# Performance work log

Measured on AMD Instinct MI355X. Metric: run time of the kernel, lower is better.

## Reference

```python
import jax, jax.numpy as jnp
from jax import lax
import numpy as np

B, C, O, K, H, W = 32, 64, 64, 3, 128, 128
COND = 16
DN = ('NCHW', 'OIHW', 'NCHW')


def setup_inputs() -> dict:
    key = jax.random.key(0)
    ks = jax.random.split(key, 12)
    def rn(k, shape, fan_in):
        return jax.random.normal(k, shape, dtype=jnp.float32) / np.sqrt(fan_in)
    return {
        "x": jax.random.normal(ks[0], (B, C, H, W), dtype=jnp.float32),
        # condition_generator: Conv2d(C,16,3,stride=2) -> pool -> relu -> Conv2d(16,16,1) -> relu
        "cg_w1": rn(ks[1], (COND, C, 3, 3), C * 9),
        "cg_b1": jnp.zeros((COND,), jnp.float32),
        "cg_w2": rn(ks[2], (COND, COND), COND),
        "cg_b2": jnp.zeros((COND,), jnp.float32),
        # weight_generator: Conv2d(16, C*K*K, 1) + ReLU
        "wg_w": rn(ks[3], (C * K * K, COND), COND),
        "wg_b": 0.1 * jax.random.normal(ks[4], (C * K * K,), dtype=jnp.float32),
        # pointwise_generator: Conv2d(16, C*O, 1) + ReLU  (channels viewed as [O, C])
        "pg_w": rn(ks[5], (C * O, COND), COND),
        "pg_b": 0.1 * jax.random.normal(ks[6], (C * O,), dtype=jnp.float32),
        # bias_generator: Conv2d(16, O, 1)
        "bg_w": rn(ks[7], (O, COND), COND),
        "bg_b": jnp.zeros((O,), jnp.float32),
        # BatchNorm2d(O) affine params (training-mode batch stats)
        "bn_gamma": jnp.ones((O,), jnp.float32),
        "bn_beta": jnp.zeros((O,), jnp.float32),
    }


def reference(x, cg_w1, cg_b1, cg_w2, cg_b2, wg_w, wg_b, pg_w, pg_b,
              bg_w, bg_b, bn_gamma, bn_beta):
    b, c, h, w = x.shape
    # ---- condition generator: conv3x3 s2 (VALID) -> global avgpool -> relu -> 1x1 -> relu
    cond = lax.conv_general_dilated(x, cg_w1, (2, 2), 'VALID', dimension_numbers=DN)
    cond = cond + cg_b1[None, :, None, None]
    cond = cond.mean(axis=(2, 3))                      # [B,16] (AdaptiveAvgPool2d(1))
    cond = jax.nn.relu(cond)
    cond = jax.nn.relu(cond @ cg_w2.T + cg_b2)         # [B,16]
    # ---- per-sample dynamic weights
    dw = jax.nn.relu(cond @ wg_w.T + wg_b).reshape(b, c, 1, K, K)   # depthwise [B,C,1,K,K]
    pw = jax.nn.relu(cond @ pg_w.T + pg_b).reshape(b, O, c)         # pointwise [B,O,C]
    dbias = cond @ bg_w.T + bg_b                                    # [B,O]
    # ---- per-sample depthwise conv (stride=1, padding=1), vmapped over batch
    def dwconv(xi, ki):  # xi [C,H,W], ki [C,1,K,K]
        return lax.conv_general_dilated(xi[None], ki, (1, 1), [(1, 1), (1, 1)],
                                        feature_group_count=c,
                                        dimension_numbers=DN)[0]
    y = jax.vmap(dwconv)(x, dw)                        # [B,C,H,W]
    # ---- per-sample pointwise 1x1 conv + dynamic bias
    out = jnp.einsum('bchw,boc->bohw', y, pw) + dbias[:, :, None, None]
    # ---- BatchNorm2d (training mode: batch statistics over N,H,W)
    mean = out.mean(axis=(0, 2, 3))
    var = out.var(axis=(0, 2, 3))
    out = (out - mean[None, :, None, None]) * lax.rsqrt(var[None, :, None, None] + 1e-5)
    out = out * bn_gamma[None, :, None, None] + bn_beta[None, :, None, None]
    return out
```

## Files before the change

kernel.cpp:

```cpp
#include <hip/hip_runtime.h>

#define B_ 32
#define C_ 64
#define O_ 64
#define H_ 128
#define W_ 128

typedef __attribute__((ext_vector_type(8))) short short8;
typedef __attribute__((ext_vector_type(4))) short short4v;
typedef __attribute__((ext_vector_type(4))) float f32x4;

typedef __attribute__((address_space(1))) const void gv_t;
typedef __attribute__((address_space(3))) void lv_t;

static __device__ __forceinline__ unsigned short f2bf(float f) {
    unsigned u = __builtin_bit_cast(unsigned, f);
    unsigned r = (u + 0x7FFFu + ((u >> 16) & 1u)) >> 16;
    return (unsigned short)r;
}

static __device__ __forceinline__ unsigned pk_bf16(float lo, float hi) {
    unsigned r;
    asm("v_cvt_pk_bf16_f32 %0, %1, %2" : "=v"(r) : "v"(lo), "v"(hi));
    return r;
}

#define WS_S      0
#define WS_COND2  18432
#define WS_DW     18944
#define WS_DBIAS  37376
#define WS_PWBF   39424
#define WS_PSUM   104960
#define WS_PSQ    236032
#define WS_SCALE  367104
#define WS_SHIFT  367168

__global__ void __launch_bounds__(256) k_strided_sums(const float* __restrict__ x,
                                                      float* __restrict__ Sout) {
    int t = threadIdx.x;
    int bc = blockIdx.x;
    const float4* xp = (const float4*)(x + (size_t)bc * (H_ * W_));
    float a[9];
#pragma unroll
    for (int k = 0; k < 9; k++) a[k] = 0.f;
#pragma unroll
    for (int k = 0; k < 16; k++) {
        int i4 = t + k * 256;
        int h = i4 >> 5;
        int w0 = (i4 & 31) << 2;
        float4 v = xp[i4];
        float mA = (w0 == 124) ? 0.f : 1.f;
        float mB = (w0 == 0) ? 0.f : 1.f;
        float rs0 = v.x + mA * v.z;
        float rs1 = v.y + mA * v.w;
        float rs2 = mB * v.x + v.z;
        float e  = (h & 1) ? 0.f : 1.f;
        float od = 1.f - e;
        float hm0 = (h == 126) ? 0.f : e;
        float hm2 = (h == 0)   ? 0.f : e;
        float hm1 = (h == 127) ? 0.f : od;
        a[0] = fmaf(hm0, rs0, a[0]); a[1] = fmaf(hm0, rs1, a[1]); a[2] = fmaf(hm0, rs2, a[2]);
        a[3] = fmaf(hm1, rs0, a[3]); a[4] = fmaf(hm1, rs1, a[4]); a[5] = fmaf(hm1, rs2, a[5]);
        a[6] = fmaf(hm2, rs0, a[6]); a[7] = fmaf(hm2, rs1, a[7]); a[8] = fmaf(hm2, rs2, a[8]);
    }
    __shared__ float red[4][9];
    int lane = t & 63, wv = t >> 6;
#pragma unroll
    for (int k = 0; k < 9; k++) {
        float v = a[k];
        for (int off = 32; off > 0; off >>= 1) v += __shfl_down(v, off);
        if (lane == 0) red[wv][k] = v;
    }
    __syncthreads();
    if (t < 9) Sout[(size_t)bc * 9 + t] = red[0][t] + red[1][t] + red[2][t] + red[3][t];
}

__global__ void __launch_bounds__(256) k_cond(const float* __restrict__ S,
                       const float* __restrict__ w1, const float* __restrict__ b1,
                       const float* __restrict__ w2, const float* __restrict__ b2,
                       float* __restrict__ cond2) {
    int b = blockIdx.x;
    int t = threadIdx.x;
    int j = t >> 4, seg = t & 15;
    const float* Sb = S + b * 576;
    const float* w1j = w1 + j * 576;
    int i0 = seg * 36;
    float s = 0.f;
#pragma unroll 4
    for (int i = 0; i < 36; i++) s = fmaf(Sb[i0 + i], w1j[i0 + i], s);
    __shared__ float red[16][16];
    __shared__ float condv[16];
    red[j][seg] = s;
    __syncthreads();
    if (t < 16) {
        float acc = 0.f;
#pragma unroll
        for (int k = 0; k < 16; k++) acc += red[t][k];
        acc = acc * (1.f / 3969.f) + b1[t];
        condv[t] = fmaxf(acc, 0.f);
    }
    __syncthreads();
    if (t < 16) {
        float s2 = b2[t];
#pragma unroll
        for (int k = 0; k < 16; k++) s2 = fmaf(condv[k], w2[t * 16 + k], s2);
        cond2[b * 16 + t] = fmaxf(s2, 0.f);
    }
}

__global__ void k_dyn(const float* __restrict__ cond2,
                      const float* __restrict__ wg_w, const float* __restrict__ wg_b,
                      const float* __restrict__ pg_w, const float* __restrict__ pg_b,
                      const float* __restrict__ bg_w, const float* __restrict__ bg_b,
                      float* __restrict__ dw, unsigned short* __restrict__ pwbf,
                      float* __restrict__ dbias) {
    int idx = blockIdx.x * 256 + threadIdx.x;
    if (idx < 18432) {
        int b = idx / 576, r = idx - b * 576;
        const float* cd = cond2 + b * 16;
        float s = wg_b[r];
#pragma unroll
        for (int j = 0; j < 16; j++) s += cd[j] * wg_w[r * 16 + j];
        dw[idx] = fmaxf(s, 0.f);
    } else if (idx < 18432 + 131072) {
        int k = idx - 18432;
        int b = k >> 12, r = k & 4095;
        const float* cd = cond2 + b * 16;
        float s = pg_b[r];
#pragma unroll
        for (int j = 0; j < 16; j++) s += cd[j] * pg_w[r * 16 + j];
        pwbf[k] = f2bf(fmaxf(s, 0.f));
    } else if (idx < 151552) {
        int k = idx - 149504;
        int b = k >> 6, r = k & 63;
        const float* cd = cond2 + b * 16;
        float s = bg_b[r];
#pragma unroll
        for (int j = 0; j < 16; j++) s += cd[j] * bg_w[r * 16 + j];
        dbias[k] = s;
    }
}

struct SM4 {
    unsigned short y[256 * 36];
    float xr[2][4][4][128];
    float dwl[64 * 12];
    float sred[4][64];
    float qred[4][64];
    float dbl[64];
};

__global__ void __launch_bounds__(256, 4) k_fused(
        const float* __restrict__ x, const float* __restrict__ dw,
        const unsigned short* __restrict__ pwbf, const float* __restrict__ dbias,
        float* __restrict__ out, float* __restrict__ psum, float* __restrict__ psq) {
    __shared__ SM4 sm;
    int t = threadIdx.x;
    int bx = blockIdx.x;
    int b = bx >> 6;
    int pt = bx & 63;
    int h0 = pt << 1;

    int l = t & 63, w_id = t >> 6;
    int quad = l >> 4, l15 = l & 15;
    int pxbase = w_id << 6;

    int m = t & 3;
    int px0 = t & ~3;
    int h_loc = px0 >> 7;
    int w0 = px0 & 127;
    float mk0 = (h0 == 0   && h_loc == 0) ? 0.f : 1.f;
    float mk2 = (h0 == 126 && h_loc == 1) ? 0.f : 1.f;

    for (int i = t; i < 576; i += 256) {
        int c = i / 9, k = i - c * 9;
        sm.dwl[c * 12 + k] = dw[b * 576 + i];
    }
    if (t < 64) sm.dbl[t] = dbias[b * 64 + t];

    const float* xb = x + ((size_t)b << 20);
    const unsigned short* pwb = pwbf + (size_t)b * 4096;

    f32x4 acc[4][4];
#pragma unroll
    for (int i = 0; i < 4; i++)
#pragma unroll
        for (int j = 0; j < 4; j++) acc[i][j] = (f32x4){0.f, 0.f, 0.f, 0.f};

    auto stage = [&](int bf, int cbg) {
#pragma unroll
        for (int k2 = 0; k2 < 2; k2++) {
            int f4 = t + k2 * 256;
            int cc = f4 >> 7, rem = f4 & 127;
            int rr = rem >> 5, w4 = rem & 31;
            int hh = h0 - 1 + rr;
            hh = hh < 0 ? 0 : (hh > 127 ? 127 : hh);
            const float* src = xb + ((size_t)(cbg + cc) << 14) + hh * 128 + (w4 << 2);
            float* dst = &sm.xr[bf][cc][rr][w4 << 2];
            __builtin_amdgcn_global_load_lds((gv_t*)src, (lv_t*)dst, 16, 0, 0);
        }
    };

    short8 bfr[4];
    auto load_bfr = [&](int hf) {
#pragma unroll
        for (int nt = 0; nt < 4; nt++) {
            int o = nt * 16 + l15;
            bfr[nt] = *(const short8*)(pwb + o * 64 + hf * 32 + quad * 8);
        }
    };

    auto domfma = [&]() {
        char* yb = (char*)sm.y;
#pragma unroll
        for (int mt = 0; mt < 4; mt++) {
            int px = pxbase + mt * 16 + l15;
            int bofs = px * 72;
            int sx = px & 7;
            short4v lo = *(short4v*)(yb + bofs + 8 * ((2 * quad)     ^ sx));
            short4v hi = *(short4v*)(yb + bofs + 8 * ((2 * quad + 1) ^ sx));
            short8 a = __builtin_shufflevector(lo, hi, 0, 1, 2, 3, 4, 5, 6, 7);
#pragma unroll
            for (int nt = 0; nt < 4; nt++)
                acc[mt][nt] = __builtin_amdgcn_mfma_f32_16x16x32_bf16(
                    a, bfr[nt], acc[mt][nt], 0, 0, 0);
        }
    };

    load_bfr(0);
    stage(0, 0);
    __syncthreads();

    int buf = 0;
#pragma unroll
    for (int idx = 0; idx < 16; idx++) {
        int cb = idx * 4;
        int rp = idx & 7;
        if (idx < 15) stage(buf ^ 1, cb + 4);

        const float* dvp = sm.dwl + (cb + m) * 12;
        float4 d0 = *(const float4*)(dvp);
        float4 d1 = *(const float4*)(dvp + 4);
        float4 d2 = *(const float4*)(dvp + 8);
        float dA0 = d0.x * mk0, dB0 = d0.y * mk0, dC0 = d0.z * mk0;
        float dA1 = d0.w,       dB1 = d1.x,       dC1 = d1.y;
        float dA2 = d1.z * mk2, dB2 = d1.w * mk2, dC2 = d2.x * mk2;
        const float* xc = &sm.xr[buf][m][0][0];
        float y0 = 0.f, y1 = 0.f, y2 = 0.f, y3 = 0.f;
#define STEN(dAx, dBx, dCx, KH) { \
        const float* row = xc + (h_loc + KH) * 128; \
        float4 fc = *(const float4*)(row + w0); \
        float4 fm = *(const float4*)(row + (w0 ? w0 - 4 : 0)); \
        float4 fp = *(const float4*)(row + ((w0 < 124) ? w0 + 4 : 120)); \
        float lft = w0 ? fm.w : 0.f; \
        float rgt = (w0 < 124) ? fp.x : 0.f; \
        y0 = fmaf(dAx, lft,  fmaf(dBx, fc.x, fmaf(dCx, fc.y, y0))); \
        y1 = fmaf(dAx, fc.x, fmaf(dBx, fc.y, fmaf(dCx, fc.z, y1))); \
        y2 = fmaf(dAx, fc.y, fmaf(dBx, fc.z, fmaf(dCx, fc.w, y2))); \
        y3 = fmaf(dAx, fc.z, fmaf(dBx, fc.w, fmaf(dCx, rgt, y3))); }
        STEN(dA0, dB0, dC0, 0)
        STEN(dA1, dB1, dC1, 1)
        STEN(dA2, dB2, dC2, 2)
#undef STEN

        unsigned p01 = pk_bf16(y0, y1);
        unsigned p23 = pk_bf16(y2, y3);
        bool mhi = (m & 2) != 0;
        bool mlo = (m & 1) != 0;
        unsigned send0 = mhi ? p01 : p23;
        unsigned keep0 = mhi ? p23 : p01;
        unsigned x2 = (unsigned)__shfl_xor((int)send0, 2);
        unsigned Lw = mhi ? x2 : keep0;
        unsigned Hw = mhi ? keep0 : x2;
        unsigned E0 = (Lw & 0xFFFFu) | (Hw << 16);
        unsigned E1 = (Lw >> 16) | (Hw & 0xFFFF0000u);
        unsigned Zk = mlo ? E1 : E0;
        unsigned Zs = mlo ? E0 : E1;
        unsigned x1 = (unsigned)__shfl_xor((int)Zs, 1);
        unsigned Aw = mlo ? x1 : Zk;
        unsigned Bw = mlo ? Zk : x1;
        unsigned w01 = (Aw & 0xFFFFu) | (Bw << 16);
        unsigned w23 = (Aw >> 16) | (Bw & 0xFFFF0000u);
        int px = px0 | m;
        int W = px * 72 + 8 * (rp ^ (px & 7));
        *(uint2*)((char*)sm.y + W) = make_uint2(w01, w23);

        __syncthreads();
        buf ^= 1;
        if (idx == 7) {
            domfma();
            __syncthreads();
            load_bfr(1);
        }
    }
    domfma();

    float* outb = out + ((size_t)b << 20);
#pragma unroll
    for (int nt = 0; nt < 4; nt++) {
        int o = nt * 16 + l15;
        float dbv = sm.dbl[o];
        float s = 0.f, q = 0.f;
        float* og = outb + (size_t)o * 16384 + h0 * 128 + pxbase + quad * 4;
#pragma unroll
        for (int mt = 0; mt < 4; mt++) {
            f32x4 a = acc[mt][nt];
            float4 v = make_float4(a.x + dbv, a.y + dbv, a.z + dbv, a.w + dbv);
            s += v.x + v.y + v.z + v.w;
            q += v.x * v.x + v.y * v.y + v.z * v.z + v.w * v.w;
            *(float4*)(og + mt * 16) = v;
        }
        s += __shfl_xor(s, 16); s += __shfl_xor(s, 32);
        q += __shfl_xor(q, 16); q += __shfl_xor(q, 32);
        if (l < 16) { sm.sred[w_id][o] = s; sm.qred[w_id][o] = q; }
    }
    __syncthreads();
    if (t < 64) {
        float S = sm.sred[0][t] + sm.sred[1][t] + sm.sred[2][t] + sm.sred[3][t];
        float Q = sm.qred[0][t] + sm.qred[1][t] + sm.qred[2][t] + sm.qred[3][t];
        psum[(size_t)bx * 64 + t] = S;
        psq[(size_t)bx * 64 + t] = Q;
    }
}

__global__ void k_bnstats(const float* __restrict__ psum, const float* __restrict__ psq,
                          const float* __restrict__ gamma, const float* __restrict__ beta,
                          float* __restrict__ scale, float* __restrict__ shift) {
    int o = blockIdx.x, t = threadIdx.x;
    float s = 0.f, q = 0.f;
    for (int i = t; i < 2048; i += 256) {
        s += psum[(size_t)i * 64 + o];
        q += psq[(size_t)i * 64 + o];
    }
    int lane = t & 63, wv = t >> 6;
    for (int off = 32; off > 0; off >>= 1) { s += __shfl_down(s, off); q += __shfl_down(q, off); }
    __shared__ float rs[4], rq[4];
    if (lane == 0) { rs[wv] = s; rq[wv] = q; }
    __syncthreads();
    if (t == 0) {
        float S = rs[0] + rs[1] + rs[2] + rs[3];
        float Q = rq[0] + rq[1] + rq[2] + rq[3];
        const float invN = 1.f / (float)(B_ * H_ * W_);
        float mean = S * invN;
        float var = fmaxf(Q * invN - mean * mean, 0.f);
        float sc = gamma[o] * rsqrtf(var + 1e-5f);
        scale[o] = sc;
        shift[o] = beta[o] - mean * sc;
    }
}

__global__ void __launch_bounds__(256) k_bnapply(float* __restrict__ out,
                          const float* __restrict__ scale, const float* __restrict__ shift) {
    __shared__ float ss[64], sh[64];
    int t = threadIdx.x;
    if (t < 64) { ss[t] = scale[t]; sh[t] = shift[t]; }
    __syncthreads();
    const int total4 = B_ * O_ * H_ * W_ / 4;
    float4* o4 = (float4*)out;
    for (int i = blockIdx.x * 256 + t; i < total4; i += gridDim.x * 256) {
        int o = (i >> 12) & 63;
        float sc = ss[o], sf = sh[o];
        float4 v = o4[i];
        v.x = fmaf(v.x, sc, sf);
        v.y = fmaf(v.y, sc, sf);
        v.z = fmaf(v.z, sc, sf);
        v.w = fmaf(v.w, sc, sf);
        o4[i] = v;
    }
}

extern "C" void kernel_launch(void* const* d_in, const int* in_sizes, int n_in,
                              void* d_out, int out_size, void* d_ws, size_t ws_size,
                              hipStream_t stream) {
    const float* x     = (const float*)d_in[0];
    const float* cg_w1 = (const float*)d_in[1];
    const float* cg_b1 = (const float*)d_in[2];
    const float* cg_w2 = (const float*)d_in[3];
    const float* cg_b2 = (const float*)d_in[4];
    const float* wg_w  = (const float*)d_in[5];
    const float* wg_b  = (const float*)d_in[6];
    const float* pg_w  = (const float*)d_in[7];
    const float* pg_b  = (const float*)d_in[8];
    const float* bg_w  = (const float*)d_in[9];
    const float* bg_b  = (const float*)d_in[10];
    const float* bn_g  = (const float*)d_in[11];
    const float* bn_b  = (const float*)d_in[12];
    float* out = (float*)d_out;
    float* ws  = (float*)d_ws;

    float* S     = ws + WS_S;
    float* cond2 = ws + WS_COND2;
    float* dw    = ws + WS_DW;
    float* dbias = ws + WS_DBIAS;
    unsigned short* pwbf = (unsigned short*)(ws + WS_PWBF);
    float* psum  = ws + WS_PSUM;
    float* psq   = ws + WS_PSQ;
    float* scale = ws + WS_SCALE;
    float* shift = ws + WS_SHIFT;

    k_strided_sums<<<B_ * C_, 256, 0, stream>>>(x, S);
    k_cond<<<B_, 256, 0, stream>>>(S, cg_w1, cg_b1, cg_w2, cg_b2, cond2);
    k_dyn<<<(151552 + 255) / 256, 256, 0, stream>>>(cond2, wg_w, wg_b, pg_w, pg_b,
                                                    bg_w, bg_b, dw, pwbf, dbias);
    k_fused<<<2048, 256, 0, stream>>>(x, dw, pwbf, dbias, out, psum, psq);
    k_bnstats<<<O_, 256, 0, stream>>>(psum, psq, bn_g, bn_b, scale, shift);
    k_bnapply<<<4096, 256, 0, stream>>>(out, scale, shift);
}
```

Measured before the change: 361.9 us.

## Deepen x staging to five-slot half-chunk ring with fine-grained waitcnt barriers

Replaces the double-buffered x staging with a five-slot ring of half-chunk (two-channel) async global-to-LDS loads, kept two to three halves ahead. Full __syncthreads calls become explicit s_waitcnt vmcnt/lgkmcnt plus s_barrier, so loads already in flight do not have to drain at every step. The bf16 y tile moves to a plain [8][256][4] layout that reuses its space for the reduction scratch, and the BN partial sums are stored transposed so the stats kernel reads them contiguously. The aim is to hide global-load latency behind the stencil work and to cut barrier stalls. In exchange, correctness now rests on hand-counted vmcnt values, and the unswizzled y layout may add LDS bank conflicts.

New measurement: 369.7 us. 2.2% more time.

```diff
diff --git a/kernel.cpp b/kernel.cpp
--- a/kernel.cpp
+++ b/kernel.cpp
@@ -24,6 +24,12 @@
     asm("v_cvt_pk_bf16_f32 %0, %1, %2" : "=v"(r) : "v"(lo), "v"(hi));
     return r;
 }
+
+#define WAIT_VM1()  asm volatile("s_waitcnt vmcnt(1) lgkmcnt(0)" ::: "memory")
+#define WAIT_VM0()  asm volatile("s_waitcnt vmcnt(0) lgkmcnt(0)" ::: "memory")
+#define WAIT_LGKM() asm volatile("s_waitcnt lgkmcnt(0)" ::: "memory")
+#define BAR()       __builtin_amdgcn_s_barrier()
+#define SCHED_PIN() __builtin_amdgcn_sched_barrier(0)
 
 #define WS_S      0
 #define WS_COND2  18432
@@ -142,11 +148,12 @@
 }
 
 struct SM4 {
-    unsigned short y[256 * 36];
-    float xr[2][4][4][128];
+    union {
+        unsigned short y[8][256][4];
+        struct { float sred[4][64]; float qred[4][64]; } r;
+    } u;
+    float xr[5][1024];
     float dwl[64 * 12];
-    float sred[4][64];
-    float qred[4][64];
     float dbl[64];
 };
 
@@ -172,12 +179,6 @@
     float mk0 = (h0 == 0   && h_loc == 0) ? 0.f : 1.f;
     float mk2 = (h0 == 126 && h_loc == 1) ? 0.f : 1.f;
 
-    for (int i = t; i < 576; i += 256) {
-        int c = i / 9, k = i - c * 9;
-        sm.dwl[c * 12 + k] = dw[b * 576 + i];
-    }
-    if (t < 64) sm.dbl[t] = dbias[b * 64 + t];
-
     const float* xb = x + ((size_t)b << 20);
     const unsigned short* pwb = pwbf + (size_t)b * 4096;
 
@@ -187,18 +188,18 @@
 #pragma unroll
         for (int j = 0; j < 4; j++) acc[i][j] = (f32x4){0.f, 0.f, 0.f, 0.f};
 
-    auto stage = [&](int bf, int cbg) {
-#pragma unroll
-        for (int k2 = 0; k2 < 2; k2++) {
-            int f4 = t + k2 * 256;
-            int cc = f4 >> 7, rem = f4 & 127;
-            int rr = rem >> 5, w4 = rem & 31;
-            int hh = h0 - 1 + rr;
-            hh = hh < 0 ? 0 : (hh > 127 ? 127 : hh);
-            const float* src = xb + ((size_t)(cbg + cc) << 14) + hh * 128 + (w4 << 2);
-            float* dst = &sm.xr[bf][cc][rr][w4 << 2];
-            __builtin_amdgcn_global_load_lds((gv_t*)src, (lv_t*)dst, 16, 0, 0);
-        }
+    float* xrp = &sm.xr[0][0];
+    auto stage_half = [&](int h) {
+        int slot = h % 5;
+        int cbase = (h >> 1) * 4 + (h & 1) * 2;
+        int cc = t >> 7;
+        int rem = t & 127;
+        int rr = rem >> 5;
+        int hh = h0 - 1 + rr;
+        hh = hh < 0 ? 0 : (hh > 127 ? 127 : hh);
+        const float* src = xb + ((size_t)(cbase + cc) << 14) + hh * 128 + ((rem & 31) << 2);
+        float* dst = xrp + slot * 1024 + t * 4;
+        __builtin_amdgcn_global_load_lds((gv_t*)src, (lv_t*)dst, 16, 0, 0);
     };
 
     short8 bfr[4];
@@ -211,14 +212,11 @@
     };
 
     auto domfma = [&]() {
-        char* yb = (char*)sm.y;
 #pragma unroll
         for (int mt = 0; mt < 4; mt++) {
             int px = pxbase + mt * 16 + l15;
-            int bofs = px * 72;
-            int sx = px & 7;
-            short4v lo = *(short4v*)(yb + bofs + 8 * ((2 * quad)     ^ sx));
-            short4v hi = *(short4v*)(yb + bofs + 8 * ((2 * quad + 1) ^ sx));
+            short4v lo = *(const short4v*)&sm.u.y[2 * quad][px][0];
+            short4v hi = *(const short4v*)&sm.u.y[2 * quad + 1][px][0];
             short8 a = __builtin_shufflevector(lo, hi, 0, 1, 2, 3, 4, 5, 6, 7);
 #pragma unroll
             for (int nt = 0; nt < 4; nt++)
@@ -228,16 +226,24 @@
     };
 
     load_bfr(0);
-    stage(0, 0);
-    __syncthreads();
-
-    int buf = 0;
+    stage_half(0); SCHED_PIN();
+    stage_half(1); SCHED_PIN();
+    stage_half(2); SCHED_PIN();
+    for (int i = t; i < 576; i += 256) {
+        int c = i / 9, k = i - c * 9;
+        sm.dwl[c * 12 + k] = dw[b * 576 + i];
+    }
+    if (t < 64) sm.dbl[t] = dbias[b * 64 + t];
+    WAIT_VM1(); BAR();
+
 #pragma unroll
     for (int idx = 0; idx < 16; idx++) {
         int cb = idx * 4;
-        int rp = idx & 7;
-        if (idx < 15) stage(buf ^ 1, cb + 4);
-
+        if (2 * idx + 3 <= 31) { stage_half(2 * idx + 3); SCHED_PIN(); }
+        if (2 * idx + 4 <= 31) { stage_half(2 * idx + 4); SCHED_PIN(); }
+
+        const int s0 = (2 * idx) % 5, s1 = (2 * idx + 1) % 5;
+        const float* xc = &sm.xr[(m >= 2) ? s1 : s0][(m & 1) << 9];
         const float* dvp = sm.dwl + (cb + m) * 12;
         float4 d0 = *(const float4*)(dvp);
         float4 d1 = *(const float4*)(dvp + 4);
@@ -245,7 +251,6 @@
         float dA0 = d0.x * mk0, dB0 = d0.y * mk0, dC0 = d0.z * mk0;
         float dA1 = d0.w,       dB1 = d1.x,       dC1 = d1.y;
         float dA2 = d1.z * mk2, dB2 = d1.w * mk2, dC2 = d2.x * mk2;
-        const float* xc = &sm.xr[buf][m][0][0];
         float y0 = 0.f, y1 = 0.f, y2 = 0.f, y3 = 0.f;
 #define STEN(dAx, dBx, dCx, KH) { \
         const float* row = xc + (h_loc + KH) * 128; \
@@ -281,20 +286,24 @@
         unsigned Bw = mlo ? Zk : x1;
         unsigned w01 = (Aw & 0xFFFFu) | (Bw << 16);
         unsigned w23 = (Aw >> 16) | (Bw & 0xFFFF0000u);
-        int px = px0 | m;
-        int W = px * 72 + 8 * (rp ^ (px & 7));
-        *(uint2*)((char*)sm.y + W) = make_uint2(w01, w23);
-
-        __syncthreads();
-        buf ^= 1;
+        *(uint2*)&sm.u.y[idx & 7][t][0] = make_uint2(w01, w23);
+
         if (idx == 7) {
+            WAIT_VM1(); BAR();
             domfma();
-            __syncthreads();
+            WAIT_LGKM(); BAR();
             load_bfr(1);
+        } else if (idx == 15) {
+            WAIT_LGKM(); BAR();
+            domfma();
+        } else if (idx == 14) {
+            WAIT_VM0(); BAR();
+        } else {
+            WAIT_VM1(); BAR();
         }
     }
-    domfma();
-
+
+    WAIT_LGKM(); BAR();
     float* outb = out + ((size_t)b << 20);
 #pragma unroll
     for (int nt = 0; nt < 4; nt++) {
@@ -312,14 +321,14 @@
         }
         s += __shfl_xor(s, 16); s += __shfl_xor(s, 32);
         q += __shfl_xor(q, 16); q += __shfl_xor(q, 32);
-        if (l < 16) { sm.sred[w_id][o] = s; sm.qred[w_id][o] = q; }
-    }
-    __syncthreads();
+        if (l < 16) { sm.u.r.sred[w_id][o] = s; sm.u.r.qred[w_id][o] = q; }
+    }
+    WAIT_LGKM(); BAR();
     if (t < 64) {
-        float S = sm.sred[0][t] + sm.sred[1][t] + sm.sred[2][t] + sm.sred[3][t];
-        float Q = sm.qred[0][t] + sm.qred[1][t] + sm.qred[2][t] + sm.qred[3][t];
-        psum[(size_t)bx * 64 + t] = S;
-        psq[(size_t)bx * 64 + t] = Q;
+        float S = sm.u.r.sred[0][t] + sm.u.r.sred[1][t] + sm.u.r.sred[2][t] + sm.u.r.sred[3][t];
+        float Q = sm.u.r.qred[0][t] + sm.u.r.qred[1][t] + sm.u.r.qred[2][t] + sm.u.r.qred[3][t];
+        psum[(size_t)t * 2048 + bx] = S;
+        psq[(size_t)t * 2048 + bx] = Q;
     }
 }
 
@@ -329,8 +338,8 @@
     int o = blockIdx.x, t = threadIdx.x;
     float s = 0.f, q = 0.f;
     for (int i = t; i < 2048; i += 256) {
-        s += psum[(size_t)i * 64 + o];
-        q += psq[(size_t)i * 64 + o];
+        s += psum[(size_t)o * 2048 + i];
+        q += psq[(size_t)o * 2048 + i];
     }
     int lane = t & 63, wv = t >> 6;
     for (int off = 32; off > 0; off >>= 1) { s += __shfl_down(s, off); q += __shfl_down(q, off); }
```
